# Performance work log

Hardware: AMD Instinct MI355X
Metric: run time of the kernel (lower is better)

The kernel has to match this reference:

```python
import jax, jax.numpy as jnp
import numpy as np
from jax import lax

# --- model/problem dims (see init_kwargs) ---
G, NPG, R, F, HID, L = 40, 500, 8, 256, 256, 3   # graphs(frames), nodes/graph, relations, feat, hidden, layers
N = G * NPG                                       # 20000 nodes
EPG = 8000
E = G * EPG                                       # 320000 edges
TOTAL = L * HID                                   # 768 = concat of layer outputs
LSTM_IN, LSTM_HID, NCLASS = 256, 256, 2
RATIO = 0.5
K = int(np.ceil(RATIO * NPG))                     # 250 nodes kept per graph by SAGPool


def setup_inputs() -> dict:
    key = jax.random.key(0)
    ks = jax.random.split(key, 16)
    s = 0.05
    x = jax.random.normal(ks[0], (N, F), dtype=jnp.float32)
    # intra-graph edges: node ids offset by graph index
    off = jnp.arange(G, dtype=jnp.int32)[:, None] * NPG
    src = jax.random.randint(ks[1], (G, EPG), 0, NPG, dtype=jnp.int32) + off
    dst = jax.random.randint(ks[2], (G, EPG), 0, NPG, dtype=jnp.int32) + off
    edge_index = jnp.stack([src.reshape(-1), dst.reshape(-1)])
    edge_attr = jax.random.randint(ks[3], (E,), 0, R, dtype=jnp.int32)
    batch = jnp.repeat(jnp.arange(G, dtype=jnp.int32), NPG)
    # RGCN layer params (layer0 in=F==HID so all layers stack)
    conv_W = jax.random.normal(ks[4], (L, R, HID, HID), dtype=jnp.float32) * s
    conv_root = jax.random.normal(ks[5], (L, HID, HID), dtype=jnp.float32) * s
    conv_bias = jnp.zeros((L, HID), dtype=jnp.float32)
    # SAGPool scorer: RGCNConv(TOTAL, 1, R)
    pool_W = jax.random.normal(ks[6], (R, TOTAL, 1), dtype=jnp.float32) * s
    pool_root = jax.random.normal(ks[7], (TOTAL, 1), dtype=jnp.float32) * s
    pool_bias = jnp.zeros((1,), dtype=jnp.float32)
    fc1_W = jax.random.normal(ks[8], (LSTM_IN, TOTAL), dtype=jnp.float32) * s
    fc1_b = jnp.zeros((LSTM_IN,), dtype=jnp.float32)
    W_ih = jax.random.normal(ks[9], (4 * LSTM_HID, LSTM_IN), dtype=jnp.float32) * s
    W_hh = jax.random.normal(ks[10], (4 * LSTM_HID, LSTM_HID), dtype=jnp.float32) * s
    b_ih = jnp.zeros((4 * LSTM_HID,), dtype=jnp.float32)
    b_hh = jnp.zeros((4 * LSTM_HID,), dtype=jnp.float32)
    fc2_W = jax.random.normal(ks[11], (NCLASS, LSTM_HID), dtype=jnp.float32) * s
    fc2_b = jnp.zeros((NCLASS,), dtype=jnp.float32)
    return dict(x=x, edge_index=edge_index, edge_attr=edge_attr, batch=batch,
                conv_W=conv_W, conv_root=conv_root, conv_bias=conv_bias,
                pool_W=pool_W, pool_root=pool_root, pool_bias=pool_bias,
                fc1_W=fc1_W, fc1_b=fc1_b, W_ih=W_ih, W_hh=W_hh, b_ih=b_ih, b_hh=b_hh,
                fc2_W=fc2_W, fc2_b=fc2_b)


def rgcn_conv(x, src, dst, etype, W, root, bias):
    """PyG (Fast)RGCNConv: per-relation mean aggregation summed over relations + root + bias."""
    num_nodes = x.shape[0]
    Rr = W.shape[0]
    h_all = jnp.einsum('ni,rio->rno', x, W)          # [R, N, out] per-relation transform
    msg = h_all[etype, src]                           # [E, out] per-edge message
    seg = dst * Rr + etype                            # (node, relation) segment id
    cnt = jax.ops.segment_sum(jnp.ones((src.shape[0],), x.dtype), seg,
                              num_segments=num_nodes * Rr)
    norm = 1.0 / jnp.maximum(cnt[seg], 1.0)           # per-(dst,rel) mean normalization
    agg = jax.ops.segment_sum(msg * norm[:, None], dst, num_segments=num_nodes)
    return agg + x @ root + bias


def lstm_scan(xs, W_ih, W_hh, b_ih, b_hh):
    """torch.nn.LSTM (single layer, batch=1) over sequence xs [T, in]; torch gate order i,f,g,o."""
    H = W_hh.shape[1]
    def step(carry, xt):
        h, c = carry
        gates = xt @ W_ih.T + h @ W_hh.T + b_ih + b_hh
        i, f, g, o = jnp.split(gates, 4)
        c = jax.nn.sigmoid(f) * c + jax.nn.sigmoid(i) * jnp.tanh(g)
        h = jax.nn.sigmoid(o) * jnp.tanh(c)
        return (h, c), h
    init = (jnp.zeros((H,), xs.dtype), jnp.zeros((H,), xs.dtype))
    (h, c), ys = lax.scan(step, init, xs)
    return ys, h


def reference(x, edge_index, edge_attr, batch,
              conv_W, conv_root, conv_bias,
              pool_W, pool_root, pool_bias,
              fc1_W, fc1_b, W_ih, W_hh, b_ih, b_hh, fc2_W, fc2_b):
    src, dst = edge_index[0], edge_index[1]
    # stacked RGCN layers, outputs concatenated (dropout omitted: eval mode)
    h = x
    outs = []
    for l in range(L):
        h = jax.nn.relu(rgcn_conv(h, src, dst, edge_attr, conv_W[l], conv_root[l], conv_bias[l]))
        outs.append(h)
    xc = jnp.concatenate(outs, axis=-1)               # [N, TOTAL]
    # SAGPool: RGCN scorer -> tanh -> per-graph top-k (batch is contiguous equal-size graphs)
    score = jnp.tanh(rgcn_conv(xc, src, dst, edge_attr, pool_W, pool_root, pool_bias).reshape(-1))
    topv, topi = lax.top_k(score.reshape(G, NPG), K)  # [G, K]
    xg = xc.reshape(G, NPG, TOTAL)
    xsel = jnp.take_along_axis(xg, topi[:, :, None], axis=1) * topv[:, :, None]
    # readout_type='mean': global_mean_pool over kept nodes per graph
    readout = xsel.mean(axis=1)                       # [G, TOTAL]
    h1 = jax.nn.relu(readout @ fc1_W.T + fc1_b)       # [G, LSTM_IN]
    # temporal_type='lstm_last': last hidden state over the G-frame sequence
    _, hlast = lstm_scan(h1, W_ih, W_hh, b_ih, b_hh)  # [LSTM_HID]
    logits = hlast @ fc2_W.T + fc2_b                  # [NCLASS]
    return jax.nn.log_softmax(logits, axis=-1)
```

## Files before the change

kernel.cpp:

```cpp
#include <hip/hip_runtime.h>

typedef unsigned short u16;
typedef short bf8 __attribute__((ext_vector_type(8)));
typedef short bf4 __attribute__((ext_vector_type(4)));
typedef float f4 __attribute__((ext_vector_type(4)));
typedef _Float16 h2v __attribute__((ext_vector_type(2)));
typedef __fp16 g2v __attribute__((ext_vector_type(2)));
typedef unsigned int u4v __attribute__((ext_vector_type(4)));

#define N_NODES 20000
#define N_EDGES 320000
#define NGRAPH 40
#define NPG 500
#define KTOP 250
#define NSEG (N_NODES * 8)

#define P_CONV_BIAS 0
#define P_POOL_W    768
#define P_POOL_ROOT 6912
#define P_POOL_BIAS 7680
#define P_FC1_W     7688
#define P_FC1_B     204296
#define P_W_IH      204552
#define P_B_IH      466696
#define P_B_HH      467720
#define P_FC2_W     468744
#define P_FC2_B     469256
#define P_TOTAL     469264

#define PR_B0 469264
#define PR_C0 (PR_B0 + 640000)
#define PR_D0 (PR_C0 + 1769472)
#define PR_END (PR_D0 + 131072)

__device__ __forceinline__ float b2f(u16 u) {
    union { unsigned int i; float f; } v; v.i = ((unsigned int)u) << 16; return v.f;
}
__device__ __forceinline__ u16 f2b(float f) {
    union { float f; unsigned int i; } v; v.f = f;
    unsigned int x = v.i;
    return (u16)((x + 0x7fffu + ((x >> 16) & 1u)) >> 16);
}
__device__ __forceinline__ float wred(float s) {
    #pragma unroll
    for (int off = 32; off > 0; off >>= 1) s += __shfl_down(s, off);
    return s;
}
__device__ __forceinline__ float fdot2u(unsigned a, unsigned b, float c) {
#if __has_builtin(__builtin_amdgcn_fdot2)
    union { unsigned u; h2v h; } ua, ub; ua.u = a; ub.u = b;
    return __builtin_amdgcn_fdot2(ua.h, ub.h, c, false);
#else
    union { unsigned u; g2v h; } ua, ub; ua.u = a; ub.u = b;
    return c + (float)ua.h[0] * (float)ub.h[0] + (float)ua.h[1] * (float)ub.h[1];
#endif
}
__device__ __forceinline__ unsigned packh2(float a, float b) {
    g2v h = __builtin_amdgcn_cvt_pkrtz(a, b);
    union { g2v h; unsigned u; } v; v.h = h; return v.u;
}
__device__ __forceinline__ float sigm_f(float x) {
    return 1.0f / (1.0f + __expf(-x));
}
__device__ __forceinline__ float tanh_f(float x) {
    return 1.0f - 2.0f / (1.0f + __expf(2.0f * x));
}

__global__ void k_init(unsigned int* __restrict__ flag, unsigned int* __restrict__ cnt,
                       unsigned int* __restrict__ ctr) {
    int i = blockIdx.x * 256 + threadIdx.x;
    if (i < 64) flag[i] = 0u;
    if (i < NSEG) { cnt[i] = 0u; ctr[i] = 0u; }
}

__global__ void k_detect1(const u16* __restrict__ xr, int n, unsigned int* __restrict__ fb) {
    unsigned int local = 0;
    for (int i = blockIdx.x * 256 + threadIdx.x; i < n; i += 64 * 256) {
        unsigned int u = xr[i];
        if (((u >> 7) & 0xFFu) == 0xFFu) local++;
    }
    local = (unsigned int)wred((float)local);
    if ((threadIdx.x & 63) == 0 && local) atomicAdd(&fb[1], local);
}

__device__ __forceinline__ u16 load_cvt(const void* src, size_t i, bool f32) {
    return f32 ? f2b(((const float*)src)[i]) : ((const u16*)src)[i];
}

__global__ void k_count(const int* __restrict__ dst, const int* __restrict__ et,
                        unsigned int* __restrict__ cnt, unsigned int* __restrict__ fb) {
    int e = blockIdx.x * 256 + threadIdx.x;
    if (e == 0) fb[0] = (fb[1] > 8u) ? 1u : 0u;
    if (e < N_EDGES) {
        unsigned d = (unsigned)dst[e]; if (d >= N_NODES) d = 0;
        unsigned r = (unsigned)et[e] & 7u;
        atomicAdd(&cnt[d * 8 + r], 1u);
    }
}

__global__ void k_scan1(const unsigned int* __restrict__ cnt, unsigned int* __restrict__ seg,
                        unsigned int* __restrict__ bsum) {
    __shared__ unsigned int s[256];
    int t = threadIdx.x, i = blockIdx.x * 256 + t;
    unsigned int v = (i < NSEG) ? cnt[i] : 0u;
    s[t] = v;
    __syncthreads();
    for (int off = 1; off < 256; off <<= 1) {
        unsigned int add = (t >= off) ? s[t - off] : 0u;
        __syncthreads();
        s[t] += add;
        __syncthreads();
    }
    if (i < NSEG) seg[i] = s[t] - v;
    if (t == 255) bsum[blockIdx.x] = s[255];
}
__global__ void k_scan2(unsigned int* __restrict__ bsum, int nb) {
    __shared__ unsigned int s[1024];
    int t = threadIdx.x;
    unsigned int v = (t < nb) ? bsum[t] : 0u;
    s[t] = v;
    __syncthreads();
    for (int off = 1; off < 1024; off <<= 1) {
        unsigned int add = (t >= off) ? s[t - off] : 0u;
        __syncthreads();
        s[t] += add;
        __syncthreads();
    }
    if (t < nb) bsum[t] = s[t] - v;
}
__global__ void k_scan3(unsigned int* __restrict__ seg, const unsigned int* __restrict__ bsum) {
    int i = blockIdx.x * 256 + threadIdx.x;
    if (i < NSEG) seg[i] += bsum[i >> 8];
    if (i == 0) seg[NSEG] = N_EDGES;
}
__global__ void k_place(const int* __restrict__ src, const int* __restrict__ dst,
                        const int* __restrict__ et, const unsigned int* __restrict__ seg,
                        unsigned int* __restrict__ ctr, const unsigned int* __restrict__ cnt,
                        unsigned int* __restrict__ skey, float* __restrict__ sw, int cap) {
    int e = blockIdx.x * 256 + threadIdx.x;
    if (e >= N_EDGES) return;
    unsigned s = (unsigned)src[e]; if (s >= N_NODES) s = 0;
    unsigned d = (unsigned)dst[e]; if (d >= N_NODES) d = 0;
    unsigned r = (unsigned)et[e] & 7u;
    unsigned key = d * 8 + r;
    unsigned pos = seg[key] + atomicAdd(&ctr[key], 1u);
    unsigned base = (d / (unsigned)cap) * (unsigned)cap;
    unsigned sl = s - base;
    if (sl >= (unsigned)cap) sl = 0u;
    skey[pos] = sl | (r << 16);
    unsigned c = cnt[key];
    sw[pos] = 1.0f / (float)(c < 1u ? 1u : c);
}

__global__ void k_prep(const void* conv_bias, const void* pool_W, const void* pool_root,
                       const void* pool_bias, const void* fc1_W, const void* fc1_b,
                       const void* W_ih, const void* b_ih, const void* b_hh,
                       const void* fc2_W, const void* fc2_b,
                       const void* __restrict__ x, const void* __restrict__ conv_W,
                       const void* __restrict__ conv_root, const void* __restrict__ W_hh,
                       u16* __restrict__ parms, u16* __restrict__ xc,
                       u16* __restrict__ Wt, unsigned int* __restrict__ whh4,
                       const unsigned int* __restrict__ flag) {
    int idx = blockIdx.x * 256 + threadIdx.x;
    bool f32 = (*flag != 0u);
    if (idx < PR_B0) {
        int i = idx;
        u16 v;
        if      (i < P_CONV_BIAS + 768)    v = load_cvt(conv_bias, i - P_CONV_BIAS, f32);
        else if (i < P_POOL_W + 6144)      v = load_cvt(pool_W,    i - P_POOL_W, f32);
        else if (i < P_POOL_ROOT + 768)    v = load_cvt(pool_root, i - P_POOL_ROOT, f32);
        else if (i < P_POOL_BIAS + 1)      v = load_cvt(pool_bias, i - P_POOL_BIAS, f32);
        else if (i < P_FC1_W && i >= P_POOL_BIAS) return;
        else if (i < P_FC1_W + 196608)     v = load_cvt(fc1_W,    i - P_FC1_W, f32);
        else if (i < P_FC1_B + 256)        v = load_cvt(fc1_b,    i - P_FC1_B, f32);
        else if (i < P_W_IH + 262144)      v = load_cvt(W_ih,     i - P_W_IH, f32);
        else if (i < P_B_IH + 1024)        v = load_cvt(b_ih,     i - P_B_IH, f32);
        else if (i < P_B_HH + 1024)        v = load_cvt(b_hh,     i - P_B_HH, f32);
        else if (i < P_FC2_W + 512)        v = load_cvt(fc2_W,    i - P_FC2_W, f32);
        else if (i < P_FC2_B + 2)          v = load_cvt(fc2_b,    i - P_FC2_B, f32);
        else return;
        parms[i] = v;
    } else if (idx < PR_C0) {
        int i = idx - PR_B0;
        int n = i >> 5, o = (i & 31) * 8;
        bf8 v;
        if (f32) {
            const float* s = (const float*)x + (size_t)n * 256 + o;
            #pragma unroll
            for (int c = 0; c < 8; ++c) v[c] = (short)f2b(s[c]);
        } else {
            v = *(const bf8*)((const u16*)x + (size_t)n * 256 + o);
        }
        *(bf8*)(xc + (size_t)n * 768 + 512 + o) = v;
    } else if (idx < PR_D0) {
        int i = idx - PR_C0;
        int kk = i & 63;
        int n = (i >> 6) & 255;
        int lc = i >> 14;
        int l = lc / 36, ck = lc % 36;
        int k = ck * 64 + kk;
        u16 v;
        if (k < 2048) {
            int r = k >> 8, ii = k & 255;
            v = load_cvt(conv_W, ((size_t)((l * 8 + r) * 256 + ii)) * 256 + n, f32);
        } else {
            int ii = k - 2048;
            v = load_cvt(conv_root, ((size_t)(l * 256 + ii)) * 256 + n, f32);
        }
        Wt[i] = v;
    } else if (idx < PR_END) {
        int i = idx - PR_D0;
        int c = i & 3, j = (i >> 2) & 1023, i4 = i >> 12;
        int i2 = i4 * 4 + c;
        float a, b;
        if (f32) {
            a = ((const float*)W_hh)[j * 256 + 2 * i2];
            b = ((const float*)W_hh)[j * 256 + 2 * i2 + 1];
        } else {
            a = b2f(((const u16*)W_hh)[j * 256 + 2 * i2]);
            b = b2f(((const u16*)W_hh)[j * 256 + 2 * i2 + 1]);
        }
        whh4[i] = packh2(a, b);
    }
}

__launch_bounds__(256, 3)
__global__ void k_layer2(const u16* __restrict__ xprev,
                         const u16* __restrict__ WtL,
                         u16* __restrict__ Hall,
                         u16* __restrict__ xcout, int colbase, int n0, int chnc) {
    __shared__ u16 As[64 * 264];
    int m0 = n0 + blockIdx.x * 64;
    int rg = blockIdx.y;
    int nend = n0 + chnc;
    int wave = threadIdx.x >> 6, lane = threadIdx.x & 63;
    int mrow = lane & 15, quad = lane >> 4;
    int nbase = wave * 64;

    {
        int row = threadIdx.x >> 2, sg = threadIdx.x & 3;
        int gm = m0 + row;
        u16* dstp = As + row * 264 + sg * 64;
        if (gm < nend) {
            const u16* srcp = xprev + (size_t)gm * 768 + sg * 64;
            #pragma unroll
            for (int c = 0; c < 8; ++c)
                *(bf8*)(dstp + c * 8) = *(const bf8*)(srcp + c * 8);
        } else {
            bf8 z = {0, 0, 0, 0, 0, 0, 0, 0};
            #pragma unroll
            for (int c = 0; c < 8; ++c) *(bf8*)(dstp + c * 8) = z;
        }
    }
    __syncthreads();

    f4 acc[4][4];
    #pragma unroll
    for (int nt = 0; nt < 4; ++nt)
        #pragma unroll
        for (int mh = 0; mh < 4; ++mh) acc[nt][mh] = (f4){0.0f, 0.0f, 0.0f, 0.0f};

    const u16* WtR = WtL + (size_t)(rg * 4) * 16384;
    #pragma unroll
    for (int c4 = 0; c4 < 4; ++c4) {
        const u16* Bck = WtR + (size_t)c4 * 16384;
        #pragma unroll
        for (int ks = 0; ks < 2; ++ks) {
            bf8 a[4];
            #pragma unroll
            for (int mh = 0; mh < 4; ++mh)
                a[mh] = *(const bf8*)(As + (mh * 16 + mrow) * 264 + c4 * 64 + ks * 32 + quad * 8);
            #pragma unroll
            for (int nt = 0; nt < 4; ++nt) {
                bf8 b = *(const bf8*)(Bck + (size_t)(nbase + nt * 16 + mrow) * 64
                                      + ks * 32 + quad * 8);
                #pragma unroll
                for (int mh = 0; mh < 4; ++mh)
                    acc[nt][mh] = __builtin_amdgcn_mfma_f32_16x16x32_bf16(a[mh], b, acc[nt][mh], 0, 0, 0);
            }
        }
    }

    __syncthreads();
    #pragma unroll
    for (int nt = 0; nt < 4; ++nt) {
        int col = nbase + nt * 16 + mrow;
        #pragma unroll
        for (int mh = 0; mh < 4; ++mh)
            #pragma unroll
            for (int v = 0; v < 4; ++v)
                As[(mh * 16 + quad * 4 + v) * 264 + col] = f2b(acc[nt][mh][v]);
    }
    __syncthreads();
    {
        int row = threadIdx.x >> 2, sg = threadIdx.x & 3;
        int gm = m0 + row;
        if (gm < nend) {
            u16* dst = (rg < 8)
                ? Hall + ((size_t)rg * chnc + (gm - n0)) * 256 + sg * 64
                : xcout + (size_t)gm * 768 + colbase + sg * 64;
            const u16* srcp = As + row * 264 + sg * 64;
            #pragma unroll
            for (int c = 0; c < 8; ++c)
                *(bf8*)(dst + c * 8) = *(const bf8*)(srcp + c * 8);
        }
    }
}

__launch_bounds__(256)
__global__ void k_gather(const unsigned int* __restrict__ seg,
                         const unsigned int* __restrict__ skey,
                         const float* __restrict__ sw,
                         const u16* __restrict__ Hall,
                         const u16* __restrict__ bias,
                         u16* __restrict__ xc, int colbase, int n0, int chnc) {
    int nl = blockIdx.x * 4 + (threadIdx.x >> 6);
    if (nl >= chnc) return;
    int n = n0 + nl;
    int lane = threadIdx.x & 63;
    int c0 = lane * 4;
    unsigned e0 = seg[n * 8], e1 = seg[n * 8 + 8];
    float a0 = 0.0f, a1 = 0.0f, a2 = 0.0f, a3 = 0.0f;
    unsigned key = 0; float w = 0.0f;
    if (e0 < e1) { key = skey[e0]; w = sw[e0]; }
    for (unsigned e = e0; e < e1;) {
        unsigned kc = key; float wc = w;
        ++e;
        if (e < e1) { key = skey[e]; w = sw[e]; }
        const u16* row = Hall + ((size_t)(kc >> 16) * chnc + (kc & 0xFFFFu)) * 256 + c0;
        bf4 v = *(const bf4*)row;
        a0 += wc * b2f((u16)v[0]);
        a1 += wc * b2f((u16)v[1]);
        a2 += wc * b2f((u16)v[2]);
        a3 += wc * b2f((u16)v[3]);
    }
    u16* xrow = xc + (size_t)n * 768 + colbase + c0;
    bf4 rv = *(const bf4*)xrow;
    float o0 = a0 + b2f((u16)rv[0]) + b2f(bias[c0 + 0]);
    float o1 = a1 + b2f((u16)rv[1]) + b2f(bias[c0 + 1]);
    float o2 = a2 + b2f((u16)rv[2]) + b2f(bias[c0 + 2]);
    float o3 = a3 + b2f((u16)rv[3]) + b2f(bias[c0 + 3]);
    bf4 o;
    o[0] = (short)f2b(o0 > 0.0f ? o0 : 0.0f);
    o[1] = (short)f2b(o1 > 0.0f ? o1 : 0.0f);
    o[2] = (short)f2b(o2 > 0.0f ? o2 : 0.0f);
    o[3] = (short)f2b(o3 > 0.0f ? o3 : 0.0f);
    *(bf4*)xrow = o;
}

__launch_bounds__(256)
__global__ void k_pool(const u16* __restrict__ xc, const u16* __restrict__ parms,
                       float* __restrict__ p, float* __restrict__ score) {
    int n = blockIdx.x * 4 + (threadIdx.x >> 6);
    if (n >= N_NODES) return;
    int lane = threadIdx.x & 63;
    const u16* xr = xc + (size_t)n * 768;
    float acc[9];
    #pragma unroll
    for (int rr = 0; rr < 9; ++rr) acc[rr] = 0.0f;
    #pragma unroll
    for (int q = 0; q < 12; ++q) {
        int f = lane + 64 * q;
        float xv = b2f(xr[f]);
        #pragma unroll
        for (int rr = 0; rr < 8; ++rr)
            acc[rr] += xv * b2f(parms[P_POOL_W + rr * 768 + f]);
        acc[8] += xv * b2f(parms[P_POOL_ROOT + f]);
    }
    #pragma unroll
    for (int rr = 0; rr < 9; ++rr) acc[rr] = wred(acc[rr]);
    if (lane == 0) {
        #pragma unroll
        for (int rr = 0; rr < 8; ++rr) p[rr * N_NODES + n] = acc[rr];
        score[n] = acc[8] + b2f(parms[P_POOL_BIAS]);
    }
}
__global__ void k_scatter_pool(const int* __restrict__ src, const int* __restrict__ dst,
                               const int* __restrict__ et, const unsigned int* __restrict__ cnt,
                               const float* __restrict__ p, float* __restrict__ score) {
    int e = blockIdx.x * 256 + threadIdx.x;
    if (e >= N_EDGES) return;
    int r = et[e] & 7;
    unsigned s = (unsigned)src[e]; if (s >= N_NODES) s = 0;
    unsigned d = (unsigned)dst[e]; if (d >= N_NODES) d = 0;
    unsigned c = cnt[d * 8 + r];
    float iv = 1.0f / (float)(c < 1u ? 1u : c);
    atomicAdd(&score[d], iv * p[r * N_NODES + s]);
}

__launch_bounds__(256)
__global__ void k_sort(const float* __restrict__ score, unsigned int* __restrict__ topidx,
                       float* __restrict__ topv) {
    __shared__ unsigned long long keys[512];
    __shared__ float vals[512];
    int g = blockIdx.x, tid = threadIdx.x;
    for (int i = tid; i < 512; i += 256) {
        unsigned long long key;
        float v = 0.0f;
        if (i < NPG) {
            v = tanhf(score[g * NPG + i]);
            unsigned int u = __float_as_uint(v);
            u = (u & 0x80000000u) ? ~u : (u | 0x80000000u);
            u = ~u;
            key = ((unsigned long long)u << 32) | (unsigned int)i;
        } else {
            key = 0xFFFFFFFFFFFFFFFFull;
        }
        keys[i] = key;
        vals[i] = v;
    }
    __syncthreads();
    for (int k = 2; k <= 512; k <<= 1)
        for (int j = k >> 1; j > 0; j >>= 1) {
            for (int i = tid; i < 512; i += 256) {
                int ixj = i ^ j;
                if (ixj > i) {
                    bool up = ((i & k) == 0);
                    unsigned long long a = keys[i], b = keys[ixj];
                    if ((a > b) == up) { keys[i] = b; keys[ixj] = a; }
                }
            }
            __syncthreads();
        }
    if (tid < KTOP) {
        int idx = (int)(keys[tid] & 511u);
        topidx[g * 256 + tid] = (unsigned)idx;
        topv[g * 256 + tid] = vals[idx];
    }
}

__launch_bounds__(256)
__global__ void k_readout(const unsigned int* __restrict__ topidx,
                          const float* __restrict__ topv,
                          const u16* __restrict__ xc, float* __restrict__ readout) {
    __shared__ unsigned int sidx[KTOP];
    __shared__ float sv[KTOP];
    __shared__ float part[256];
    int g = blockIdx.x, cb = blockIdx.y;
    int tid = threadIdx.x;
    if (tid < KTOP) { sidx[tid] = topidx[g * 256 + tid]; sv[tid] = topv[g * 256 + tid]; }
    __syncthreads();
    int fl = tid & 63, ng = tid >> 6;
    int f = cb * 64 + fl;
    float acc = 0.0f;
    for (int j = ng; j < KTOP; j += 4)
        acc += sv[j] * b2f(xc[(size_t)(g * NPG + sidx[j]) * 768 + f]);
    part[tid] = acc;
    __syncthreads();
    if (tid < 64) {
        float s = part[tid] + part[64 + tid] + part[128 + tid] + part[192 + tid];
        readout[(size_t)g * 768 + cb * 64 + tid] = s * (1.0f / (float)KTOP);
    }
}

__global__ void k_fc1(const float* __restrict__ readout, const u16* __restrict__ parms,
                      float* __restrict__ h1) {
    int wid = blockIdx.x * 4 + (threadIdx.x >> 6);
    if (wid >= NGRAPH * 256) return;
    int g = wid >> 8, o = wid & 255, lane = threadIdx.x & 63;
    const float* rr = readout + (size_t)g * 768;
    const u16* w = parms + P_FC1_W + (size_t)o * 768;
    float s = 0.0f;
    #pragma unroll
    for (int q = 0; q < 12; ++q) { int f = lane + 64 * q; s += rr[f] * b2f(w[f]); }
    s = wred(s);
    if (lane == 0) { s += b2f(parms[P_FC1_B + o]); h1[g * 256 + o] = s > 0.0f ? s : 0.0f; }
}
__global__ void k_gx(const float* __restrict__ h1, const u16* __restrict__ parms,
                     float* __restrict__ gx) {
    int wid = blockIdx.x * 4 + (threadIdx.x >> 6);
    if (wid >= NGRAPH * 1024) return;
    int t = wid >> 10, j = wid & 1023, lane = threadIdx.x & 63;
    const float* xr = h1 + t * 256;
    const u16* w = parms + P_W_IH + (size_t)j * 256;
    float s = 0.0f;
    #pragma unroll
    for (int q = 0; q < 4; ++q) { int f = lane + 64 * q; s += xr[f] * b2f(w[f]); }
    s = wred(s);
    if (lane == 0) gx[t * 1024 + j] = s + b2f(parms[P_B_IH + j]) + b2f(parms[P_B_HH + j]);
}

__launch_bounds__(512, 1)
__global__ void k_lstm(const float* __restrict__ gx, const unsigned int* __restrict__ whh4,
                       const u16* __restrict__ parms, void* __restrict__ out,
                       const unsigned int* __restrict__ flag) {
    __shared__ float hs[256];
    __shared__ unsigned int hs2[128];
    __shared__ float gs[1024];
    __shared__ float red[2];
    int tid = threadIdx.x;
    int j0 = tid, j1 = tid + 512;
    u4v wa[24], wb[24];
    #pragma unroll
    for (int q = 0; q < 24; ++q) {
        wa[q] = *(const u4v*)(whh4 + (((size_t)q * 1024) + j0) * 4);
        wb[q] = *(const u4v*)(whh4 + (((size_t)q * 1024) + j1) * 4);
    }
    asm volatile("" : "+v"(wa[0]), "+v"(wa[1]), "+v"(wa[2]), "+v"(wa[3]),
                      "+v"(wa[4]), "+v"(wa[5]), "+v"(wa[6]), "+v"(wa[7]),
                      "+v"(wa[8]), "+v"(wa[9]), "+v"(wa[10]), "+v"(wa[11]),
                      "+v"(wa[12]), "+v"(wa[13]), "+v"(wa[14]), "+v"(wa[15]),
                      "+v"(wa[16]), "+v"(wa[17]), "+v"(wa[18]), "+v"(wa[19]),
                      "+v"(wa[20]), "+v"(wa[21]), "+v"(wa[22]), "+v"(wa[23]));
    asm volatile("" : "+v"(wb[0]), "+v"(wb[1]), "+v"(wb[2]), "+v"(wb[3]),
                      "+v"(wb[4]), "+v"(wb[5]), "+v"(wb[6]), "+v"(wb[7]),
                      "+v"(wb[8]), "+v"(wb[9]), "+v"(wb[10]), "+v"(wb[11]),
                      "+v"(wb[12]), "+v"(wb[13]), "+v"(wb[14]), "+v"(wb[15]),
                      "+v"(wb[16]), "+v"(wb[17]), "+v"(wb[18]), "+v"(wb[19]),
                      "+v"(wb[20]), "+v"(wb[21]), "+v"(wb[22]), "+v"(wb[23]));
    if (tid < 256) hs[tid] = 0.0f;
    if (tid < 128) hs2[tid] = 0u;
    float c = 0.0f;
    __syncthreads();
    for (int t = 0; t < NGRAPH; ++t) {
        float g0 = gx[t * 1024 + j0];
        float g1 = gx[t * 1024 + j1];
        #pragma unroll
        for (int q = 0; q < 24; ++q) {
            #pragma unroll
            for (int cc = 0; cc < 4; ++cc) {
                unsigned h2 = hs2[q * 4 + cc];
                g0 = fdot2u(wa[q][cc], h2, g0);
                g1 = fdot2u(wb[q][cc], h2, g1);
            }
        }
        #pragma unroll 2
        for (int q = 24; q < 32; ++q) {
            u4v v0 = *(const u4v*)(whh4 + (((size_t)q * 1024) + j0) * 4);
            u4v v1 = *(const u4v*)(whh4 + (((size_t)q * 1024) + j1) * 4);
            #pragma unroll
            for (int cc = 0; cc < 4; ++cc) {
                unsigned h2 = hs2[q * 4 + cc];
                g0 = fdot2u(v0[cc], h2, g0);
                g1 = fdot2u(v1[cc], h2, g1);
            }
        }
        gs[j0] = g0;
        gs[j1] = g1;
        __syncthreads();
        if (tid < 256) {
            float gi = sigm_f(gs[tid]);
            float gf = sigm_f(gs[256 + tid]);
            float gg = tanh_f(gs[512 + tid]);
            float go = sigm_f(gs[768 + tid]);
            c = gf * c + gi * gg;
            float h = go * tanh_f(c);
            hs[tid] = h;
            float ho = __shfl(h, (tid & 63) ^ 1);
            if (!(tid & 1)) hs2[tid >> 1] = packh2(h, ho);
        }
        __syncthreads();
    }
    if (tid < 128) {
        int cls = tid >> 6, lane = tid & 63;
        float s = 0.0f;
        #pragma unroll
        for (int q = 0; q < 4; ++q) {
            int d = lane + 64 * q;
            s += hs[d] * b2f(parms[P_FC2_W + cls * 256 + d]);
        }
        s = wred(s);
        if (lane == 0) red[cls] = s + b2f(parms[P_FC2_B + cls]);
    }
    __syncthreads();
    if (tid == 0) {
        float l0 = red[0], l1 = red[1];
        float m = fmaxf(l0, l1);
        float lse = m + logf(expf(l0 - m) + expf(l1 - m));
        float o0 = l0 - lse, o1 = l1 - lse;
        if (*flag) { ((float*)out)[0] = o0; ((float*)out)[1] = o1; }
        else       { ((u16*)out)[0] = f2b(o0); ((u16*)out)[1] = f2b(o1); }
    }
}

struct WS {
    unsigned int* flag; unsigned int* cnt; unsigned int* seg; unsigned int* ctr;
    unsigned int* skey; float* sw; unsigned int* bsum;
    u16* Wt2; u16* xc; u16* Hall; float* p; float* score;
    unsigned int* topidx; float* topv; float* readout; float* h1;
    float* gx; unsigned int* whh4; u16* parms;
    size_t need;
};
static WS plan(char* base, int cap) {
    WS w; size_t off = 0;
    auto take = [&](size_t bytes) -> char* {
        char* p = base + off; off += (bytes + 255) & ~(size_t)255; return p;
    };
    w.flag    = (unsigned int*)take(256);
    w.cnt     = (unsigned int*)take((size_t)NSEG * 4);
    w.seg     = (unsigned int*)take((size_t)(NSEG + 1) * 4);
    w.skey    = (unsigned int*)take((size_t)N_EDGES * 4);
    w.sw      = (float*)take((size_t)N_EDGES * 4);
    w.Wt2     = (u16*)take((size_t)3 * 36 * 256 * 64 * 2);
    w.xc      = (u16*)take((size_t)N_NODES * 768 * 2);
    w.Hall    = (u16*)take((size_t)8 * cap * 256 * 2);
    w.p       = (float*)take((size_t)8 * N_NODES * 4);
    w.score   = (float*)take((size_t)N_NODES * 4);
    w.topidx  = (unsigned int*)take((size_t)NGRAPH * 256 * 4);
    w.topv    = (float*)take((size_t)NGRAPH * 256 * 4);
    w.readout = (float*)take((size_t)NGRAPH * 768 * 4);
    w.h1      = (float*)take((size_t)NGRAPH * 256 * 4);
    w.gx      = (float*)take((size_t)NGRAPH * 1024 * 4);
    w.whh4    = (unsigned int*)take((size_t)32 * 1024 * 4 * 4);
    w.parms   = (u16*)take((size_t)P_TOTAL * 2);
    w.ctr  = (unsigned int*)w.p;
    w.bsum = (unsigned int*)w.score;
    w.need = off;
    return w;
}

extern "C" void kernel_launch(void* const* d_in, const int* in_sizes, int n_in,
                              void* d_out, int out_size, void* d_ws, size_t ws_size,
                              hipStream_t stream) {
    (void)in_sizes; (void)n_in; (void)out_size;
    const void* x        = d_in[0];
    const int* edge_index= (const int*)d_in[1];
    const int* edge_attr = (const int*)d_in[2];
    const void* conv_W   = d_in[4];
    const void* conv_root= d_in[5];
    const void* conv_bias= d_in[6];
    const void* pool_W   = d_in[7];
    const void* pool_root= d_in[8];
    const void* pool_bias= d_in[9];
    const void* fc1_W    = d_in[10];
    const void* fc1_b    = d_in[11];
    const void* W_ih     = d_in[12];
    const void* W_hh     = d_in[13];
    const void* b_ih     = d_in[14];
    const void* b_hh     = d_in[15];
    const void* fc2_W    = d_in[16];
    const void* fc2_b    = d_in[17];

    const int* e_src = edge_index;
    const int* e_dst = edge_index + N_EDGES;

    if (ws_size == 0) ws_size = (size_t)64 << 20;
    int cap = 500;
    {
        const int ladder[8] = {20000, 10000, 5000, 4000, 2500, 2000, 1000, 500};
        for (int i = 0; i < 8; ++i) {
            if (plan((char*)d_ws, ladder[i]).need <= ws_size) { cap = ladder[i]; break; }
        }
    }
    WS w = plan((char*)d_ws, cap);

    k_init<<<(NSEG + 255) / 256, 256, 0, stream>>>(w.flag, w.cnt, w.ctr);
    k_detect1<<<64, 256, 0, stream>>>((const u16*)x, 1 << 18, w.flag);
    k_count<<<1250, 256, 0, stream>>>(e_dst, edge_attr, w.cnt, w.flag);
    k_scan1<<<625, 256, 0, stream>>>(w.cnt, w.seg, w.bsum);
    k_scan2<<<1, 1024, 0, stream>>>(w.bsum, 625);
    k_scan3<<<(NSEG + 255) / 256, 256, 0, stream>>>(w.seg, w.bsum);
    k_place<<<1250, 256, 0, stream>>>(e_src, e_dst, edge_attr, w.seg, w.ctr, w.cnt,
                                      w.skey, w.sw, cap);

    k_prep<<<(PR_END + 255) / 256, 256, 0, stream>>>(
        conv_bias, pool_W, pool_root, pool_bias, fc1_W, fc1_b,
        W_ih, b_ih, b_hh, fc2_W, fc2_b,
        x, conv_W, conv_root, W_hh,
        w.parms, w.xc, w.Wt2, w.whh4, w.flag);

    for (int l = 0; l < 3; ++l) {
        const u16* xprev = w.xc + (l == 0 ? 512 : (l - 1) * 256);
        const u16* WtL = w.Wt2 + (size_t)l * 36 * 16384;
        const u16* bias = w.parms + P_CONV_BIAS + l * 256;
        for (int n0 = 0; n0 < N_NODES; n0 += cap) {
            int chnc = N_NODES - n0 < cap ? N_NODES - n0 : cap;
            int tiles = (chnc + 63) / 64;
            k_layer2<<<dim3(tiles, 9), 256, 0, stream>>>(xprev, WtL, w.Hall,
                                                         w.xc, l * 256, n0, chnc);
            k_gather<<<(chnc + 3) / 4, 256, 0, stream>>>(w.seg, w.skey, w.sw, w.Hall,
                                                         bias, w.xc, l * 256, n0, chnc);
        }
    }

    k_pool<<<5000, 256, 0, stream>>>(w.xc, w.parms, w.p, w.score);
    k_scatter_pool<<<1250, 256, 0, stream>>>(e_src, e_dst, edge_attr, w.cnt, w.p, w.score);
    k_sort<<<NGRAPH, 256, 0, stream>>>(w.score, w.topidx, w.topv);
    k_readout<<<dim3(NGRAPH, 12), 256, 0, stream>>>(w.topidx, w.topv, w.xc, w.readout);
    k_fc1<<<2560, 256, 0, stream>>>(w.readout, w.parms, w.h1);
    k_gx<<<10240, 256, 0, stream>>>(w.h1, w.parms, w.gx);
    k_lstm<<<1, 512, 0, stream>>>(w.gx, w.whh4, w.parms, d_out, w.flag);
}
```

Before: 682.8 us.

## Replace atomic pool scatter with CSR segmented gather and register-broadcast LSTM state

The SAGPool score aggregation stops using per-edge atomicAdd. It now walks the precomputed destination-sorted segments (seg/skey) already built for the RGCN gather, with one thread per (node, relation) and a shuffle reduction across the 8 relations. The LSTM recurrence reads packed h values through readlane from two per-lane registers instead of repeated shared-memory loads, and the sort uses the fast tanh approximation. The gather path depends on the skey encoding and the chunk base (cap) matching the layer gather, and tanh_f may slightly change top-k ordering.

```diff
diff --git a/kernel.cpp b/kernel.cpp
--- a/kernel.cpp
+++ b/kernel.cpp
@@ -375,17 +375,27 @@
         score[n] = acc[8] + b2f(parms[P_POOL_BIAS]);
     }
 }
-__global__ void k_scatter_pool(const int* __restrict__ src, const int* __restrict__ dst,
-                               const int* __restrict__ et, const unsigned int* __restrict__ cnt,
-                               const float* __restrict__ p, float* __restrict__ score) {
-    int e = blockIdx.x * 256 + threadIdx.x;
-    if (e >= N_EDGES) return;
-    int r = et[e] & 7;
-    unsigned s = (unsigned)src[e]; if (s >= N_NODES) s = 0;
-    unsigned d = (unsigned)dst[e]; if (d >= N_NODES) d = 0;
-    unsigned c = cnt[d * 8 + r];
-    float iv = 1.0f / (float)(c < 1u ? 1u : c);
-    atomicAdd(&score[d], iv * p[r * N_NODES + s]);
+
+__launch_bounds__(256)
+__global__ void k_score(const unsigned int* __restrict__ seg,
+                        const unsigned int* __restrict__ skey,
+                        const unsigned int* __restrict__ cnt,
+                        const float* __restrict__ p, float* __restrict__ score, int cap) {
+    int key = blockIdx.x * 256 + threadIdx.x;
+    int d = key >> 3, r = key & 7;
+    unsigned base = ((unsigned)d / (unsigned)cap) * (unsigned)cap;
+    unsigned e0 = seg[key], e1 = seg[key + 1];
+    float s = 0.0f;
+    for (unsigned e = e0; e < e1; ++e) {
+        unsigned k2 = skey[e];
+        s += p[(size_t)(k2 >> 16) * N_NODES + base + (k2 & 0xFFFFu)];
+    }
+    unsigned c = cnt[key];
+    s *= 1.0f / (float)(c < 1u ? 1u : c);
+    s += __shfl_xor(s, 1);
+    s += __shfl_xor(s, 2);
+    s += __shfl_xor(s, 4);
+    if (r == 0) score[d] += s;
 }
 
 __launch_bounds__(256)
@@ -398,7 +408,7 @@
         unsigned long long key;
         float v = 0.0f;
         if (i < NPG) {
-            v = tanhf(score[g * NPG + i]);
+            v = tanh_f(score[g * NPG + i]);
             unsigned int u = __float_as_uint(v);
             u = (u & 0x80000000u) ? ~u : (u | 0x80000000u);
             u = ~u;
@@ -490,6 +500,7 @@
     __shared__ float red[2];
     int tid = threadIdx.x;
     int j0 = tid, j1 = tid + 512;
+    int lane = tid & 63;
     u4v wa[24], wb[24];
     #pragma unroll
     for (int q = 0; q < 24; ++q) {
@@ -511,6 +522,7 @@
     if (tid < 256) hs[tid] = 0.0f;
     if (tid < 128) hs2[tid] = 0u;
     float c = 0.0f;
+    int hr0 = 0, hr1 = 0;
     __syncthreads();
     for (int t = 0; t < NGRAPH; ++t) {
         float g0 = gx[t * 1024 + j0];
@@ -519,7 +531,9 @@
         for (int q = 0; q < 24; ++q) {
             #pragma unroll
             for (int cc = 0; cc < 4; ++cc) {
-                unsigned h2 = hs2[q * 4 + cc];
+                int j = q * 4 + cc;
+                unsigned h2 = (unsigned)__builtin_amdgcn_readlane(
+                                  (j < 64) ? hr0 : hr1, j & 63);
                 g0 = fdot2u(wa[q][cc], h2, g0);
                 g1 = fdot2u(wb[q][cc], h2, g1);
             }
@@ -530,7 +544,7 @@
             u4v v1 = *(const u4v*)(whh4 + (((size_t)q * 1024) + j1) * 4);
             #pragma unroll
             for (int cc = 0; cc < 4; ++cc) {
-                unsigned h2 = hs2[q * 4 + cc];
+                unsigned h2 = (unsigned)__builtin_amdgcn_readlane(hr1, q * 4 + cc - 64);
                 g0 = fdot2u(v0[cc], h2, g0);
                 g1 = fdot2u(v1[cc], h2, g1);
             }
@@ -550,17 +564,19 @@
             if (!(tid & 1)) hs2[tid >> 1] = packh2(h, ho);
         }
         __syncthreads();
+        hr0 = (int)hs2[lane];
+        hr1 = (int)hs2[64 + lane];
     }
     if (tid < 128) {
-        int cls = tid >> 6, lane = tid & 63;
+        int cls = tid >> 6, l = tid & 63;
         float s = 0.0f;
         #pragma unroll
         for (int q = 0; q < 4; ++q) {
-            int d = lane + 64 * q;
+            int d = l + 64 * q;
             s += hs[d] * b2f(parms[P_FC2_W + cls * 256 + d]);
         }
         s = wred(s);
-        if (lane == 0) red[cls] = s + b2f(parms[P_FC2_B + cls]);
+        if (l == 0) red[cls] = s + b2f(parms[P_FC2_B + cls]);
     }
     __syncthreads();
     if (tid == 0) {
@@ -674,7 +690,7 @@
     }
 
     k_pool<<<5000, 256, 0, stream>>>(w.xc, w.parms, w.p, w.score);
-    k_scatter_pool<<<1250, 256, 0, stream>>>(e_src, e_dst, edge_attr, w.cnt, w.p, w.score);
+    k_score<<<625, 256, 0, stream>>>(w.seg, w.skey, w.cnt, w.p, w.score, cap);
     k_sort<<<NGRAPH, 256, 0, stream>>>(w.score, w.topidx, w.topv);
     k_readout<<<dim3(NGRAPH, 12), 256, 0, stream>>>(w.topidx, w.topv, w.xc, w.readout);
     k_fc1<<<2560, 256, 0, stream>>>(w.readout, w.parms, w.h1);
```

Result: no change. 678.1 us (-0.7%).
